# Optimization experiments

Hardware: AMD Instinct MI355X
Metric: run time of the kernel (lower is better)

## Reference

```python
import jax, jax.numpy as jnp
import numpy as np

HIDDEN = 32
IN_DIM = 4
WARMUP = 29  # steps using ground-truth input; afterwards feed back own output


def _gru_cell(x, h, w_ih, w_hh, b_ih, b_hh):
    # PyTorch GRUCell math. x: [B, 4], h: [B, 32]
    gi = x @ w_ih.T + b_ih          # [B, 96]
    gh = h @ w_hh.T + b_hh          # [B, 96]
    i_r, i_z, i_n = jnp.split(gi, 3, axis=-1)
    h_r, h_z, h_n = jnp.split(gh, 3, axis=-1)
    r = jax.nn.sigmoid(i_r + h_r)
    z = jax.nn.sigmoid(i_z + h_z)
    n = jnp.tanh(i_n + r * h_n)
    return (1.0 - z) * n + z * h


def setup_inputs() -> dict:
    key = jax.random.key(0)
    ks = jax.random.split(key, 8)
    B, T = 131072, 60
    s_ih = 1.0 / np.sqrt(HIDDEN)
    return {
        "input": jax.random.normal(ks[0], (B, IN_DIM, T), dtype=jnp.float32),
        "w_ih": jax.random.uniform(ks[1], (3 * HIDDEN, IN_DIM), jnp.float32, -s_ih, s_ih),
        "w_hh": jax.random.uniform(ks[2], (3 * HIDDEN, HIDDEN), jnp.float32, -s_ih, s_ih),
        "b_ih": jax.random.uniform(ks[3], (3 * HIDDEN,), jnp.float32, -s_ih, s_ih),
        "b_hh": jax.random.uniform(ks[4], (3 * HIDDEN,), jnp.float32, -s_ih, s_ih),
        "w_lin": jax.random.uniform(ks[5], (IN_DIM, HIDDEN), jnp.float32, -s_ih, s_ih),
        "b_lin": jax.random.uniform(ks[6], (IN_DIM,), jnp.float32, -s_ih, s_ih),
    }


def reference(input, w_ih, w_hh, b_ih, b_hh, w_lin, b_lin):
    B, _, T = input.shape
    xs = jnp.transpose(input, (2, 0, 1))  # [T, B, 4]
    h0 = jnp.zeros((B, HIDDEN), dtype=input.dtype)
    out0 = jnp.zeros((B, IN_DIM), dtype=input.dtype)

    def step(carry, xi):
        h, prev_out, h28 = carry
        x_t, i = xi
        inp = jnp.where(i < WARMUP, x_t, prev_out)
        h = _gru_cell(inp, h, w_ih, w_hh, b_ih, b_hh)
        out = h @ w_lin.T + b_lin
        h28 = jnp.where(i == WARMUP - 1, h, h28)
        return (h, out, h28), out

    (_, _, h28), outs = jax.lax.scan(step, (h0, out0, h0), (xs, jnp.arange(T)))
    outputs = jnp.transpose(outs, (1, 2, 0))  # [B, 4, T] to match torch.stack(dim=2)
    return outputs, [h28]
```

## Files before the change

kernel.cpp:

```cpp
#include <hip/hip_runtime.h>

#define T_STEPS 60
#define WARMUP  29
#define HID     32
#define CT      240

__device__ __forceinline__ float fexp2(float x) { return __builtin_amdgcn_exp2f(x); }
__device__ __forceinline__ float frcp(float x)  { return __builtin_amdgcn_rcpf(x); }
__device__ __forceinline__ float sigmoid_f(float x) {
    return frcp(1.0f + fexp2(-1.4426950408889634f * x));
}
__device__ __forceinline__ float tanh_f(float x) {
    float e = fexp2(2.8853900817779268f * x);
    return 1.0f - 2.0f * frcp(e + 1.0f);
}

template<int K>
__device__ __forceinline__ float bcast(float x) {
    return __int_as_float(__builtin_amdgcn_ds_swizzle(__float_as_int(x), (K << 5)));
}

#define GATHER32(v, x) do { \
    v[0]  = bcast<0>(x);  v[1]  = bcast<1>(x);  v[2]  = bcast<2>(x);  v[3]  = bcast<3>(x);  \
    v[4]  = bcast<4>(x);  v[5]  = bcast<5>(x);  v[6]  = bcast<6>(x);  v[7]  = bcast<7>(x);  \
    v[8]  = bcast<8>(x);  v[9]  = bcast<9>(x);  v[10] = bcast<10>(x); v[11] = bcast<11>(x); \
    v[12] = bcast<12>(x); v[13] = bcast<13>(x); v[14] = bcast<14>(x); v[15] = bcast<15>(x); \
    v[16] = bcast<16>(x); v[17] = bcast<17>(x); v[18] = bcast<18>(x); v[19] = bcast<19>(x); \
    v[20] = bcast<20>(x); v[21] = bcast<21>(x); v[22] = bcast<22>(x); v[23] = bcast<23>(x); \
    v[24] = bcast<24>(x); v[25] = bcast<25>(x); v[26] = bcast<26>(x); v[27] = bcast<27>(x); \
    v[28] = bcast<28>(x); v[29] = bcast<29>(x); v[30] = bcast<30>(x); v[31] = bcast<31>(x); \
} while (0)

#define GRU_STEP() do {                                                        \
    float gr = bgr, gz = bgz, gni = bgni, gnh = bgnh;                          \
    _Pragma("unroll")                                                          \
    for (int c = 0; c < 4; ++c) {                                              \
        gr  = __builtin_fmaf(wir[c], u[c], gr);                                \
        gz  = __builtin_fmaf(wiz[c], u[c], gz);                                \
        gni = __builtin_fmaf(win[c], u[c], gni);                               \
    }                                                                          \
    _Pragma("unroll")                                                          \
    for (int k = 0; k < HID; ++k) {                                            \
        gr  = __builtin_fmaf(whr[k], v[k], gr);                                \
        gz  = __builtin_fmaf(whz[k], v[k], gz);                                \
        gnh = __builtin_fmaf(whn[k], v[k], gnh);                               \
    }                                                                          \
    float r = sigmoid_f(gr);                                                   \
    float z = sigmoid_f(gz);                                                   \
    float n = tanh_f(__builtin_fmaf(r, gnh, gni));                             \
    x = __builtin_fmaf(z, x - n, n);                                           \
    GATHER32(v, x);                                                            \
    o = bl;                                                                    \
    _Pragma("unroll")                                                          \
    for (int k = 0; k < HID; ++k) o = __builtin_fmaf(wlr[k], v[k], o);         \
} while (0)

__global__ __launch_bounds__(256, 2) void gru_fused(
    const float* __restrict__ in,
    const float* __restrict__ w_ih,  const float* __restrict__ w_hh,
    const float* __restrict__ b_ih,  const float* __restrict__ b_hh,
    const float* __restrict__ w_lin, const float* __restrict__ b_lin,
    float* __restrict__ out, float* __restrict__ h28out, int B)
{
    const int lane = threadIdx.x & 63;
    const int j    = lane & 31;
    const int wv   = threadIdx.x >> 6;
    const int s    = lane >> 5;
    const int b    = blockIdx.x * 8 + wv * 2 + s;

    float whr[HID], whz[HID], whn[HID], wlr[HID];
    float wir[4], wiz[4], win[4];
    {
        const float4* pr = (const float4*)(w_hh + (size_t)j * HID);
        const float4* pz = (const float4*)(w_hh + (size_t)(HID + j) * HID);
        const float4* pn = (const float4*)(w_hh + (size_t)(2 * HID + j) * HID);
        const float4* pl = (const float4*)(w_lin + (size_t)(j & 3) * HID);
#pragma unroll
        for (int q = 0; q < 8; ++q) {
            float4 a = pr[q];
            whr[4*q] = a.x; whr[4*q+1] = a.y; whr[4*q+2] = a.z; whr[4*q+3] = a.w;
            float4 c = pz[q];
            whz[4*q] = c.x; whz[4*q+1] = c.y; whz[4*q+2] = c.z; whz[4*q+3] = c.w;
            float4 d = pn[q];
            whn[4*q] = d.x; whn[4*q+1] = d.y; whn[4*q+2] = d.z; whn[4*q+3] = d.w;
            float4 e = pl[q];
            wlr[4*q] = e.x; wlr[4*q+1] = e.y; wlr[4*q+2] = e.z; wlr[4*q+3] = e.w;
        }
        float4 a = ((const float4*)w_ih)[j];
        wir[0] = a.x; wir[1] = a.y; wir[2] = a.z; wir[3] = a.w;
        float4 c = ((const float4*)w_ih)[HID + j];
        wiz[0] = c.x; wiz[1] = c.y; wiz[2] = c.z; wiz[3] = c.w;
        float4 d = ((const float4*)w_ih)[2 * HID + j];
        win[0] = d.x; win[1] = d.y; win[2] = d.z; win[3] = d.w;
    }
    const float bgr  = b_ih[j]           + b_hh[j];
    const float bgz  = b_ih[HID + j]     + b_hh[HID + j];
    const float bgni = b_ih[2 * HID + j];
    const float bgnh = b_hh[2 * HID + j];
    const float bl   = b_lin[j & 3];

    float v[HID], u[4];
    float x = 0.0f, o = 0.0f;
#pragma unroll
    for (int k = 0; k < HID; ++k) v[k] = 0.0f;

    const float* pin  = in  + (size_t)b * CT;
    float*       pout = out + (size_t)b * CT + (j & 3) * T_STEPS;

#pragma unroll 1
    for (int t = 0; t < WARMUP; ++t) {
        u[0] = pin[t];
        u[1] = pin[60 + t];
        u[2] = pin[120 + t];
        u[3] = pin[180 + t];
        GRU_STEP();
        if (j < 4) pout[t] = o;
    }

    h28out[(size_t)b * HID + j] = x;

#pragma unroll 1
    for (int t = WARMUP; t < T_STEPS; ++t) {
        u[0] = bcast<0>(o);
        u[1] = bcast<1>(o);
        u[2] = bcast<2>(o);
        u[3] = bcast<3>(o);
        GRU_STEP();
        if (j < 4) pout[t] = o;
    }
}

extern "C" void kernel_launch(void* const* d_in, const int* in_sizes, int n_in,
                              void* d_out, int out_size, void* d_ws, size_t ws_size,
                              hipStream_t stream) {
    const float* input = (const float*)d_in[0];
    const float* w_ih  = (const float*)d_in[1];
    const float* w_hh  = (const float*)d_in[2];
    const float* b_ih  = (const float*)d_in[3];
    const float* b_hh  = (const float*)d_in[4];
    const float* w_lin = (const float*)d_in[5];
    const float* b_lin = (const float*)d_in[6];

    const int B = in_sizes[0] / CT;
    float* out = (float*)d_out;
    float* h28 = out + (size_t)B * CT;
    (void)d_ws; (void)ws_size;

    hipLaunchKernelGGL(gru_fused, dim3(B / 8), dim3(256), 0, stream,
                       input, w_ih, w_hh, b_ih, b_hh, w_lin, b_lin, out, h28, B);
}
```

Measured before the change: 1.588 ms.

## Process two batch rows per 32-lane group to reuse register-held weights

Each 32-lane half-wave now advances two independent batch sequences at once, interleaving their gate FMAs, activations and broadcasts. The register-resident weight rows are reused across both sequences, and two dependency chains give the scheduler independent work to hide swizzle and transcendental latency. The grid is halved and the launch-bounds occupancy hint is dropped. In exchange the extra state vectors roughly double the per-thread activation registers, which may lower occupancy or cause spills.

```diff
diff --git a/kernel.cpp b/kernel.cpp
--- a/kernel.cpp
+++ b/kernel.cpp
@@ -20,42 +20,57 @@
     return __int_as_float(__builtin_amdgcn_ds_swizzle(__float_as_int(x), (K << 5)));
 }
 
-#define GATHER32(v, x) do { \
-    v[0]  = bcast<0>(x);  v[1]  = bcast<1>(x);  v[2]  = bcast<2>(x);  v[3]  = bcast<3>(x);  \
-    v[4]  = bcast<4>(x);  v[5]  = bcast<5>(x);  v[6]  = bcast<6>(x);  v[7]  = bcast<7>(x);  \
-    v[8]  = bcast<8>(x);  v[9]  = bcast<9>(x);  v[10] = bcast<10>(x); v[11] = bcast<11>(x); \
-    v[12] = bcast<12>(x); v[13] = bcast<13>(x); v[14] = bcast<14>(x); v[15] = bcast<15>(x); \
-    v[16] = bcast<16>(x); v[17] = bcast<17>(x); v[18] = bcast<18>(x); v[19] = bcast<19>(x); \
-    v[20] = bcast<20>(x); v[21] = bcast<21>(x); v[22] = bcast<22>(x); v[23] = bcast<23>(x); \
-    v[24] = bcast<24>(x); v[25] = bcast<25>(x); v[26] = bcast<26>(x); v[27] = bcast<27>(x); \
-    v[28] = bcast<28>(x); v[29] = bcast<29>(x); v[30] = bcast<30>(x); v[31] = bcast<31>(x); \
+#define GATHER32(vv, xx) do { \
+    vv[0]  = bcast<0>(xx);  vv[1]  = bcast<1>(xx);  vv[2]  = bcast<2>(xx);  vv[3]  = bcast<3>(xx);  \
+    vv[4]  = bcast<4>(xx);  vv[5]  = bcast<5>(xx);  vv[6]  = bcast<6>(xx);  vv[7]  = bcast<7>(xx);  \
+    vv[8]  = bcast<8>(xx);  vv[9]  = bcast<9>(xx);  vv[10] = bcast<10>(xx); vv[11] = bcast<11>(xx); \
+    vv[12] = bcast<12>(xx); vv[13] = bcast<13>(xx); vv[14] = bcast<14>(xx); vv[15] = bcast<15>(xx); \
+    vv[16] = bcast<16>(xx); vv[17] = bcast<17>(xx); vv[18] = bcast<18>(xx); vv[19] = bcast<19>(xx); \
+    vv[20] = bcast<20>(xx); vv[21] = bcast<21>(xx); vv[22] = bcast<22>(xx); vv[23] = bcast<23>(xx); \
+    vv[24] = bcast<24>(xx); vv[25] = bcast<25>(xx); vv[26] = bcast<26>(xx); vv[27] = bcast<27>(xx); \
+    vv[28] = bcast<28>(xx); vv[29] = bcast<29>(xx); vv[30] = bcast<30>(xx); vv[31] = bcast<31>(xx); \
 } while (0)
 
-#define GRU_STEP() do {                                                        \
-    float gr = bgr, gz = bgz, gni = bgni, gnh = bgnh;                          \
+#define GRU_STEP2() do {                                                       \
+    float grA = bgr, gzA = bgz, gniA = bgni, gnhA = bgnh;                      \
+    float grB = bgr, gzB = bgz, gniB = bgni, gnhB = bgnh;                      \
     _Pragma("unroll")                                                          \
     for (int c = 0; c < 4; ++c) {                                              \
-        gr  = __builtin_fmaf(wir[c], u[c], gr);                                \
-        gz  = __builtin_fmaf(wiz[c], u[c], gz);                                \
-        gni = __builtin_fmaf(win[c], u[c], gni);                               \
+        grA  = __builtin_fmaf(wir[c], ua[c], grA);                             \
+        grB  = __builtin_fmaf(wir[c], ub[c], grB);                             \
+        gzA  = __builtin_fmaf(wiz[c], ua[c], gzA);                             \
+        gzB  = __builtin_fmaf(wiz[c], ub[c], gzB);                             \
+        gniA = __builtin_fmaf(win[c], ua[c], gniA);                            \
+        gniB = __builtin_fmaf(win[c], ub[c], gniB);                            \
     }                                                                          \
     _Pragma("unroll")                                                          \
     for (int k = 0; k < HID; ++k) {                                            \
-        gr  = __builtin_fmaf(whr[k], v[k], gr);                                \
-        gz  = __builtin_fmaf(whz[k], v[k], gz);                                \
-        gnh = __builtin_fmaf(whn[k], v[k], gnh);                               \
+        grA  = __builtin_fmaf(whr[k], va[k], grA);                             \
+        grB  = __builtin_fmaf(whr[k], vb[k], grB);                             \
+        gzA  = __builtin_fmaf(whz[k], va[k], gzA);                             \
+        gzB  = __builtin_fmaf(whz[k], vb[k], gzB);                             \
+        gnhA = __builtin_fmaf(whn[k], va[k], gnhA);                            \
+        gnhB = __builtin_fmaf(whn[k], vb[k], gnhB);                            \
     }                                                                          \
-    float r = sigmoid_f(gr);                                                   \
-    float z = sigmoid_f(gz);                                                   \
-    float n = tanh_f(__builtin_fmaf(r, gnh, gni));                             \
-    x = __builtin_fmaf(z, x - n, n);                                           \
-    GATHER32(v, x);                                                            \
-    o = bl;                                                                    \
+    float rA = sigmoid_f(grA);                                                 \
+    float rB = sigmoid_f(grB);                                                 \
+    float zA = sigmoid_f(gzA);                                                 \
+    float zB = sigmoid_f(gzB);                                                 \
+    float nA = tanh_f(__builtin_fmaf(rA, gnhA, gniA));                         \
+    float nB = tanh_f(__builtin_fmaf(rB, gnhB, gniB));                         \
+    xa = __builtin_fmaf(zA, xa - nA, nA);                                      \
+    xb = __builtin_fmaf(zB, xb - nB, nB);                                      \
+    GATHER32(va, xa);                                                          \
+    GATHER32(vb, xb);                                                          \
+    oa = bl; ob = bl;                                                          \
     _Pragma("unroll")                                                          \
-    for (int k = 0; k < HID; ++k) o = __builtin_fmaf(wlr[k], v[k], o);         \
+    for (int k = 0; k < HID; ++k) {                                            \
+        oa = __builtin_fmaf(wlr[k], va[k], oa);                                \
+        ob = __builtin_fmaf(wlr[k], vb[k], ob);                                \
+    }                                                                          \
 } while (0)
 
-__global__ __launch_bounds__(256, 2) void gru_fused(
+__global__ __launch_bounds__(256) void gru_fused(
     const float* __restrict__ in,
     const float* __restrict__ w_ih,  const float* __restrict__ w_hh,
     const float* __restrict__ b_ih,  const float* __restrict__ b_hh,
@@ -66,7 +81,8 @@
     const int j    = lane & 31;
     const int wv   = threadIdx.x >> 6;
     const int s    = lane >> 5;
-    const int b    = blockIdx.x * 8 + wv * 2 + s;
+    const int bA   = blockIdx.x * 16 + wv * 4 + s * 2;
+    const int bB   = bA + 1;
 
     float whr[HID], whz[HID], whn[HID], wlr[HID];
     float wir[4], wiz[4], win[4];
@@ -99,34 +115,37 @@
     const float bgnh = b_hh[2 * HID + j];
     const float bl   = b_lin[j & 3];
 
-    float v[HID], u[4];
-    float x = 0.0f, o = 0.0f;
+    float va[HID], vb[HID], ua[4], ub[4];
+    float xa = 0.0f, xb = 0.0f, oa = 0.0f, ob = 0.0f;
 #pragma unroll
-    for (int k = 0; k < HID; ++k) v[k] = 0.0f;
+    for (int k = 0; k < HID; ++k) { va[k] = 0.0f; vb[k] = 0.0f; }
 
-    const float* pin  = in  + (size_t)b * CT;
-    float*       pout = out + (size_t)b * CT + (j & 3) * T_STEPS;
+    const float* pinA  = in  + (size_t)bA * CT;
+    const float* pinB  = in  + (size_t)bB * CT;
+    float*       poutA = out + (size_t)bA * CT + (j & 3) * T_STEPS;
+    float*       poutB = out + (size_t)bB * CT + (j & 3) * T_STEPS;
 
 #pragma unroll 1
     for (int t = 0; t < WARMUP; ++t) {
-        u[0] = pin[t];
-        u[1] = pin[60 + t];
-        u[2] = pin[120 + t];
-        u[3] = pin[180 + t];
-        GRU_STEP();
-        if (j < 4) pout[t] = o;
+        ua[0] = pinA[t];       ub[0] = pinB[t];
+        ua[1] = pinA[60 + t];  ub[1] = pinB[60 + t];
+        ua[2] = pinA[120 + t]; ub[2] = pinB[120 + t];
+        ua[3] = pinA[180 + t]; ub[3] = pinB[180 + t];
+        GRU_STEP2();
+        if (j < 4) { poutA[t] = oa; poutB[t] = ob; }
     }
 
-    h28out[(size_t)b * HID + j] = x;
+    h28out[(size_t)bA * HID + j] = xa;
+    h28out[(size_t)bB * HID + j] = xb;
 
 #pragma unroll 1
     for (int t = WARMUP; t < T_STEPS; ++t) {
-        u[0] = bcast<0>(o);
-        u[1] = bcast<1>(o);
-        u[2] = bcast<2>(o);
-        u[3] = bcast<3>(o);
-        GRU_STEP();
-        if (j < 4) pout[t] = o;
+        ua[0] = bcast<0>(oa);  ub[0] = bcast<0>(ob);
+        ua[1] = bcast<1>(oa);  ub[1] = bcast<1>(ob);
+        ua[2] = bcast<2>(oa);  ub[2] = bcast<2>(ob);
+        ua[3] = bcast<3>(oa);  ub[3] = bcast<3>(ob);
+        GRU_STEP2();
+        if (j < 4) { poutA[t] = oa; poutB[t] = ob; }
     }
 }
 
@@ -146,6 +165,6 @@
     float* h28 = out + (size_t)B * CT;
     (void)d_ws; (void)ws_size;
 
-    hipLaunchKernelGGL(gru_fused, dim3(B / 8), dim3(256), 0, stream,
+    hipLaunchKernelGGL(gru_fused, dim3(B / 16), dim3(256), 0, stream,
                        input, w_ih, w_hh, b_ih, b_hh, w_lin, b_lin, out, h28, B);
 }
```

Measured after the change: 2.123 ms. +33.7%, slower.
